# Performance work log

Hardware: AMD Instinct MI355X
Metric: run time of the kernel (lower is better)

Reference implementation:

```python
import jax, jax.numpy as jnp
import numpy as np

N, C_IN, C_OUT, K = 100000, 64, 64, 16
E = N * K
BN_EPS = 1e-5


def setup_inputs() -> dict:
    key = jax.random.key(0)
    ks = jax.random.split(key, 4)
    x = jax.random.normal(ks[0], (N, C_IN), dtype=jnp.float32)
    # knn-style edge list: each node i is the center (row) of exactly K edges
    edge_row = jnp.repeat(jnp.arange(N, dtype=jnp.int64), K)
    edge_col = jax.random.randint(ks[1], (E,), 0, N).astype(jnp.int64)
    W1 = jax.random.normal(ks[2], (2 * C_IN, C_OUT), dtype=jnp.float32) * (1.0 / np.sqrt(2 * C_IN))
    W2 = jax.random.normal(ks[3], (C_OUT, C_OUT), dtype=jnp.float32) * (1.0 / np.sqrt(C_OUT))
    return {
        'x': x, 'edge_row': edge_row, 'edge_col': edge_col,
        'W1': W1, 'b1': jnp.zeros((C_OUT,), jnp.float32),
        'g1': jnp.ones((C_OUT,), jnp.float32), 'be1': jnp.zeros((C_OUT,), jnp.float32),
        'W2': W2, 'b2': jnp.zeros((C_OUT,), jnp.float32),
        'g2': jnp.ones((C_OUT,), jnp.float32), 'be2': jnp.zeros((C_OUT,), jnp.float32),
    }


def _bn(h, gamma, beta):
    # BatchNorm1d in training mode: biased batch stats over the edge dim
    mean = jnp.mean(h, axis=0)
    var = jnp.mean(jnp.square(h - mean), axis=0)
    return (h - mean) * jax.lax.rsqrt(var + BN_EPS) * gamma + beta


def reference(x, edge_row, edge_col, W1, b1, g1, be1, W2, b2, g2, be2):
    xi = x[edge_row]                      # [E, C_in]  gather (center)
    xj = x[edge_col]                      # [E, C_in]  gather (neighbor)
    feat = jnp.concatenate([xi, xj - xi], axis=1)   # [E, 2*C_in]
    h = jax.nn.relu(_bn(feat @ W1 + b1, g1, be1))   # [E, C_out]
    h = jax.nn.relu(_bn(h @ W2 + b2, g2, be2))      # [E, C_out]
    # scatter-max back to nodes; every node has K edges so no empty segments
    out = jax.ops.segment_max(h, edge_row, num_segments=x.shape[0])
    return out
```

## Files before the change

### kernel.cpp

```cpp
#include <hip/hip_runtime.h>


#define N_NODES 100000
#define KE 16
#define E_EDGES (N_NODES * KE)
#define BN_EPS 1e-5f
#define NCHUNK (N_NODES / KE)
#define GSLOTS 16

typedef __attribute__((ext_vector_type(8))) short bf16x8;
typedef __attribute__((ext_vector_type(4))) float f32x4;
typedef __attribute__((ext_vector_type(4))) int i32x4;

#define MFMA(a, b, c) __builtin_amdgcn_mfma_f32_16x16x32_bf16((a), (b), (c), 0, 0, 0)

static __device__ __forceinline__ short bf16b(float f) {
  __bf16 h = (__bf16)f;
  return __builtin_bit_cast(short, h);
}

#if __has_builtin(__builtin_amdgcn_cvt_pk_bf16_f32)
static __device__ __forceinline__ int pk2(float a, float b) {
  return __builtin_bit_cast(int, __builtin_amdgcn_cvt_pk_bf16_f32(a, b));
}
#else
static __device__ __forceinline__ int pk2(float a, float b) {
  return (int)(unsigned short)bf16b(a) | ((int)(unsigned short)bf16b(b) << 16);
}
#endif

static __device__ __forceinline__ bf16x8 pack8(float4 a, float4 b) {
  i32x4 v = {pk2(a.x, a.y), pk2(a.z, a.w), pk2(b.x, b.y), pk2(b.z, b.w)};
  return __builtin_bit_cast(bf16x8, v);
}

static __device__ __forceinline__ float bf2f(short s) {
  unsigned u = ((unsigned)(unsigned short)s) << 16;
  return __builtin_bit_cast(float, u);
}

__global__ __launch_bounds__(256) void k_prep(const float* __restrict__ x,
                                              short* __restrict__ xb,
                                              const float* __restrict__ W1,
                                              const float* __restrict__ W2,
                                              short* __restrict__ wp1,
                                              short* __restrict__ wp2,
                                              float* __restrict__ gaccz) {
  if (blockIdx.x < 3125) {
    int g = blockIdx.x * 256 + threadIdx.x;
    const float4* x4 = (const float4*)x;
    float4 f0 = x4[2 * g], f1 = x4[2 * g + 1];
    *(bf16x8*)(xb + g * 8) = pack8(f0, f1);
    return;
  }
  if (blockIdx.x == 3131) {
    float4 z = {0.f, 0.f, 0.f, 0.f};
    for (int i = 0; i < 4; i++)
      ((float4*)gaccz)[threadIdx.x * 4 + i] = z;
    return;
  }
  int tid = (blockIdx.x - 3125) * 256 + threadIdx.x;
  if (tid < 1024) {
    int l = tid & 63, st = tid >> 6;
    int s = st >> 2, t = st & 3;
    int quad = l >> 4, n16 = l & 15;
    for (int j = 0; j < 8; j++) {
      int k = 32 * s + quad * 8 + j, c = 16 * t + n16;
      float w = (s < 2) ? (W1[k * 64 + c] - W1[(k + 64) * 64 + c])
                        : W1[k * 64 + c];
      wp1[tid * 8 + j] = bf16b(w);
    }
  } else if (tid < 1536) {
    int e = tid - 1024;
    int l = e & 63, st = e >> 6;
    int s = st >> 2, t = st & 3;
    int quad = l >> 4, n16 = l & 15;
    for (int j = 0; j < 8; j++) {
      int k = 32 * s + quad * 8 + j, c = 16 * t + n16;
      wp2[e * 8 + j] = bf16b(W2[k * 64 + c]);
    }
  }
}

static __device__ __forceinline__ void stat_acc(const f32x4 acc[4], float sacc[4],
                                                float qacc[4]) {
#pragma unroll
  for (int t = 0; t < 4; t++) {
    sacc[t] += (acc[t][0] + acc[t][1]) + (acc[t][2] + acc[t][3]);
    qacc[t] = fmaf(acc[t][0], acc[t][0],
              fmaf(acc[t][1], acc[t][1],
              fmaf(acc[t][2], acc[t][2],
              fmaf(acc[t][3], acc[t][3], qacc[t]))));
  }
}

static __device__ __forceinline__ void stat_flush(float sacc[4], float qacc[4],
                                                  int quad, int n16, float* lstat) {
#pragma unroll
  for (int t = 0; t < 4; t++) {
    float s = sacc[t], q = qacc[t];
    s += __shfl_xor(s, 16); s += __shfl_xor(s, 32);
    q += __shfl_xor(q, 16); q += __shfl_xor(q, 32);
    if (quad == 0) {
      atomicAdd(&lstat[16 * t + n16], s);
      atomicAdd(&lstat[64 + 16 * t + n16], q);
    }
  }
}

static __device__ __forceinline__ void bn_finalize(const float* __restrict__ gacc,
                                                   const float* __restrict__ g,
                                                   const float* __restrict__ be,
                                                   float* lbn, int tid) {
  if (tid < 64) {
    float s = 0.f, q = 0.f;
#pragma unroll
    for (int i = 0; i < GSLOTS; i++) {
      s += gacc[i * 128 + tid];
      q += gacc[i * 128 + 64 + tid];
    }
    float mean = s * (1.0f / E_EDGES);
    float var = q * (1.0f / E_EDGES) - mean * mean;
    float rstd = rsqrtf(var + BN_EPS);
    float a = g[tid] * rstd;
    lbn[tid] = a;
    lbn[64 + tid] = be[tid] - mean * a;
  }
}

static __device__ __forceinline__ void compute_y(const short* __restrict__ xisrc,
                                                 const short* wfl,
                                                 float* yt, int l, int quad, int n16) {
  bf16x8 a0 = *(const bf16x8*)(&xisrc[n16 * 64 + quad * 8]);
  bf16x8 a1 = *(const bf16x8*)(&xisrc[n16 * 64 + 32 + quad * 8]);
  const bf16x8* wf = (const bf16x8*)wfl;
#pragma unroll
  for (int t = 0; t < 4; t++) {
    f32x4 y = {0.f, 0.f, 0.f, 0.f};
    y = MFMA(a0, wf[(0 + t) * 64 + l], y);
    y = MFMA(a1, wf[(4 + t) * 64 + l], y);
#pragma unroll
    for (int r = 0; r < 4; r++)
      yt[(quad * 4 + r) * 64 + 16 * t + n16] = y[r];
  }
}

__global__ __launch_bounds__(256, 4) void k_pass1(const short* __restrict__ xb,
                                                  const int* __restrict__ ecol,
                                                  const bf16x8* __restrict__ wp1,
                                                  float* __restrict__ gacc) {
  __shared__ float lstat[128];
  __shared__ float yt[1024];
  __shared__ __align__(16) short wfl[8192];
  int tid = threadIdx.x;
  if (tid < 128) lstat[tid] = 0.f;
  int nb = blockIdx.x * 16;
  int wave = tid >> 6, l = tid & 63, quad = l >> 4, n16 = l & 15;
  int idx[4];
#pragma unroll
  for (int v = 0; v < 4; v++)
    idx[v] = ecol[nb * KE + (wave * 4 + v) * 16 + n16];
  bf16x8 j0[4], j1[4];
#pragma unroll
  for (int v = 0; v < 4; v++) {
    const short* pj = xb + (size_t)idx[v] * 64 + quad * 8;
    j0[v] = *(const bf16x8*)pj;
    j1[v] = *(const bf16x8*)(pj + 32);
  }
#pragma unroll
  for (int r = 0; r < 4; r++)
    ((bf16x8*)wfl)[r * 256 + tid] = wp1[r * 256 + tid];
  __syncthreads();
  const bf16x8* wf = (const bf16x8*)wfl;
  if (wave == 0) compute_y(xb + (size_t)nb * 64, wfl, yt, l, quad, n16);
  __syncthreads();
  float sacc[4] = {0.f, 0.f, 0.f, 0.f}, qacc[4] = {0.f, 0.f, 0.f, 0.f};
#pragma unroll
  for (int v = 0; v < 4; v++) {
    int p = wave * 4 + v;
    f32x4 acc[4];
#pragma unroll
    for (int t = 0; t < 4; t++) {
      float yv = yt[p * 64 + 16 * t + n16];
      f32x4 a = {yv, yv, yv, yv};
      a = MFMA(j0[v], wf[(8 + t) * 64 + l], a);
      a = MFMA(j1[v], wf[(12 + t) * 64 + l], a);
      acc[t] = a;
    }
    stat_acc(acc, sacc, qacc);
  }
  stat_flush(sacc, qacc, quad, n16, lstat);
  __syncthreads();
  if (tid < 128)
    atomicAdd(&gacc[(blockIdx.x & (GSLOTS - 1)) * 128 + tid], lstat[tid]);
}

__global__ __launch_bounds__(256, 4) void k_pass2(const short* __restrict__ xb,
                                                  const int* __restrict__ ecol,
                                                  const bf16x8* __restrict__ wp1,
                                                  const bf16x8* __restrict__ wp2,
                                                  const float* __restrict__ gacc1,
                                                  const float* __restrict__ g1,
                                                  const float* __restrict__ be1,
                                                  float* __restrict__ gacc,
                                                  short* __restrict__ hmax,
                                                  short* __restrict__ hmin) {
  __shared__ float lstat[128];
  __shared__ float lbn[128];
  __shared__ float yt[1024];
  __shared__ __align__(16) short wfl[8192];
  __shared__ __align__(16) short tiles[4][16 * 72];
  int tid = threadIdx.x;
  if (tid < 128) lstat[tid] = 0.f;
  bn_finalize(gacc1, g1, be1, lbn, tid);
  int nb = blockIdx.x * 16;
  int wave = tid >> 6, l = tid & 63, quad = l >> 4, n16 = l & 15;
  int idx[4];
#pragma unroll
  for (int v = 0; v < 4; v++)
    idx[v] = ecol[nb * KE + (wave * 4 + v) * 16 + n16];
  bf16x8 j0[4], j1[4];
#pragma unroll
  for (int v = 0; v < 4; v++) {
    const short* pj = xb + (size_t)idx[v] * 64 + quad * 8;
    j0[v] = *(const bf16x8*)pj;
    j1[v] = *(const bf16x8*)(pj + 32);
  }
#pragma unroll
  for (int r = 0; r < 4; r++)
    ((bf16x8*)wfl)[r * 256 + tid] = wp1[r * 256 + tid];
  const bf16x8* wf = (const bf16x8*)wfl;
  bf16x8 wf2[8];
#pragma unroll
  for (int u = 0; u < 8; u++) wf2[u] = wp2[u * 64 + l];
  __syncthreads();
  float a1c[4], b1c[4];
#pragma unroll
  for (int t = 0; t < 4; t++) {
    a1c[t] = lbn[16 * t + n16];
    b1c[t] = lbn[64 + 16 * t + n16];
  }
  if (wave == 0) compute_y(xb + (size_t)nb * 64, wfl, yt, l, quad, n16);
  __syncthreads();
  float sacc[4] = {0.f, 0.f, 0.f, 0.f}, qacc[4] = {0.f, 0.f, 0.f, 0.f};
  short* myt = &tiles[wave][0];
#pragma unroll
  for (int v = 0; v < 4; v++) {
    int p = wave * 4 + v;
    f32x4 acc1[4];
#pragma unroll
    for (int t = 0; t < 4; t++) {
      float yv = yt[p * 64 + 16 * t + n16];
      f32x4 a = {yv, yv, yv, yv};
      a = MFMA(j0[v], wf[(8 + t) * 64 + l], a);
      a = MFMA(j1[v], wf[(12 + t) * 64 + l], a);
      acc1[t] = a;
    }
#pragma unroll
    for (int t = 0; t < 4; t++) {
      int c = 16 * t + n16;
#pragma unroll
      for (int r = 0; r < 4; r++) {
        float h = fmaxf(fmaf(acc1[t][r], a1c[t], b1c[t]), 0.f);
        myt[(quad * 4 + r) * 72 + c] = bf16b(h);
      }
    }
    bf16x8 f0 = *(bf16x8*)(myt + n16 * 72 + quad * 8);
    bf16x8 f1 = *(bf16x8*)(myt + n16 * 72 + 32 + quad * 8);
    f32x4 acc2[4];
#pragma unroll
    for (int t = 0; t < 4; t++) {
      f32x4 a = {0.f, 0.f, 0.f, 0.f};
      a = MFMA(f0, wf2[0 + t], a);
      a = MFMA(f1, wf2[4 + t], a);
      acc2[t] = a;
    }
    stat_acc(acc2, sacc, qacc);
    float vmx[4], vmn[4];
#pragma unroll
    for (int t = 0; t < 4; t++) {
      float mx = fmaxf(fmaxf(acc2[t][0], acc2[t][1]), fmaxf(acc2[t][2], acc2[t][3]));
      float mn = fminf(fminf(acc2[t][0], acc2[t][1]), fminf(acc2[t][2], acc2[t][3]));
      mx = fmaxf(mx, __shfl_xor(mx, 16)); mx = fmaxf(mx, __shfl_xor(mx, 32));
      mn = fminf(mn, __shfl_xor(mn, 16)); mn = fminf(mn, __shfl_xor(mn, 32));
      vmx[t] = mx; vmn[t] = mn;
    }
    int n = nb + p;
    float ox = (quad == 0) ? vmx[0] : (quad == 1) ? vmx[1] : (quad == 2) ? vmx[2] : vmx[3];
    float on = (quad == 0) ? vmn[0] : (quad == 1) ? vmn[1] : (quad == 2) ? vmn[2] : vmn[3];
    hmax[(size_t)n * 64 + l] = bf16b(ox);
    hmin[(size_t)n * 64 + l] = bf16b(on);
  }
  stat_flush(sacc, qacc, quad, n16, lstat);
  __syncthreads();
  if (tid < 128)
    atomicAdd(&gacc[(blockIdx.x & (GSLOTS - 1)) * 128 + tid], lstat[tid]);
}

__global__ __launch_bounds__(256) void k_pass3(const short* __restrict__ hmax,
                                               const short* __restrict__ hmin,
                                               const float* __restrict__ gacc2,
                                               const float* __restrict__ g2,
                                               const float* __restrict__ be2,
                                               float* __restrict__ out) {
  __shared__ float lbn[128];
  int tid = threadIdx.x;
  bn_finalize(gacc2, g2, be2, lbn, tid);
  __syncthreads();
  int g = blockIdx.x * 256 + tid;
  int base = g * 4;
  int c4 = base & 63;
  short4 mx4 = *(const short4*)(hmax + base);
  short4 mn4 = *(const short4*)(hmin + base);
  float4 a4 = *(const float4*)(&lbn[c4]);
  float4 b4 = *(const float4*)(&lbn[64 + c4]);
  float4 o;
  o.x = fmaxf(a4.x >= 0.f ? fmaf(a4.x, bf2f(mx4.x), b4.x) : fmaf(a4.x, bf2f(mn4.x), b4.x), 0.f);
  o.y = fmaxf(a4.y >= 0.f ? fmaf(a4.y, bf2f(mx4.y), b4.y) : fmaf(a4.y, bf2f(mn4.y), b4.y), 0.f);
  o.z = fmaxf(a4.z >= 0.f ? fmaf(a4.z, bf2f(mx4.z), b4.z) : fmaf(a4.z, bf2f(mn4.z), b4.z), 0.f);
  o.w = fmaxf(a4.w >= 0.f ? fmaf(a4.w, bf2f(mx4.w), b4.w) : fmaf(a4.w, bf2f(mn4.w), b4.w), 0.f);
  *(float4*)(out + base) = o;
}

extern "C" void kernel_launch(void* const* d_in, const int* in_sizes, int n_in,
                              void* d_out, int out_size, void* d_ws, size_t ws_size,
                              hipStream_t stream) {
  const float* x   = (const float*)d_in[0];
  const int*   ec  = (const int*)d_in[2];
  const float* W1  = (const float*)d_in[3];
  const float* g1  = (const float*)d_in[5];
  const float* be1 = (const float*)d_in[6];
  const float* W2  = (const float*)d_in[7];
  const float* g2  = (const float*)d_in[9];
  const float* be2 = (const float*)d_in[10];
  float* out = (float*)d_out;

  char* ws = (char*)d_ws;
  bf16x8* wp1  = (bf16x8*)(ws);
  bf16x8* wp2  = (bf16x8*)(ws + 16384);
  float* gacc1 = (float*)(ws + 24576);
  float* gacc2 = (float*)(ws + 32768);
  short* xb    = (short*)(ws + 98304);
  short* hmax  = (short*)(ws + 98304 + 12800000);
  short* hmin  = (short*)(ws + 98304 + 2 * 12800000);

  hipLaunchKernelGGL(k_prep, dim3(3132), dim3(256), 0, stream, x, xb,
                     W1, W2, (short*)wp1, (short*)wp2, gacc1);
  hipLaunchKernelGGL(k_pass1, dim3(NCHUNK), dim3(256), 0, stream,
                     xb, ec, wp1, gacc1);
  hipLaunchKernelGGL(k_pass2, dim3(NCHUNK), dim3(256), 0, stream,
                     xb, ec, wp1, wp2, gacc1, g1, be1, gacc2, hmax, hmin);
  hipLaunchKernelGGL(k_pass3, dim3(6250), dim3(256), 0, stream,
                     hmax, hmin, gacc2, g2, be2, out);
}
```

Before: 219.3 us.

## Precompute per-node first-layer projections Y and Z, gather projections instead of features

Splits the first linear layer by linearity: each node's contributions Y = x·(W1a−W1b) in fp32 and Z = x·W1b in bf16 are computed once per node in a new kernel. The edge pre-activation then becomes Y[row] + Z[col], so the two edge passes no longer run first-layer MFMAs or stage W1 in shared memory. Pass 1 reduces to an elementwise add plus sum and sum-of-squares statistics, and pass 2 applies batch norm directly to the gathered Z. The cost is an extra kernel and larger intermediates (fp32 Y, bf16 Z), and rounding Z to bf16 after the matmul changes numerics slightly.

```diff
diff --git a/kernel.cpp b/kernel.cpp
--- a/kernel.cpp
+++ b/kernel.cpp
@@ -6,6 +6,7 @@
 #define E_EDGES (N_NODES * KE)
 #define BN_EPS 1e-5f
 #define NCHUNK (N_NODES / KE)
+#define NTILES (N_NODES / 16)
 #define GSLOTS 16
 
 typedef __attribute__((ext_vector_type(8))) short bf16x8;
@@ -34,32 +35,28 @@
   return __builtin_bit_cast(bf16x8, v);
 }
 
+static __device__ __forceinline__ bf16x8 pack8f(const float h[8]) {
+  i32x4 v = {pk2(h[0], h[1]), pk2(h[2], h[3]), pk2(h[4], h[5]), pk2(h[6], h[7])};
+  return __builtin_bit_cast(bf16x8, v);
+}
+
 static __device__ __forceinline__ float bf2f(short s) {
   unsigned u = ((unsigned)(unsigned short)s) << 16;
   return __builtin_bit_cast(float, u);
 }
 
-__global__ __launch_bounds__(256) void k_prep(const float* __restrict__ x,
-                                              short* __restrict__ xb,
-                                              const float* __restrict__ W1,
+__global__ __launch_bounds__(256) void k_prep(const float* __restrict__ W1,
                                               const float* __restrict__ W2,
                                               short* __restrict__ wp1,
                                               short* __restrict__ wp2,
                                               float* __restrict__ gaccz) {
-  if (blockIdx.x < 3125) {
-    int g = blockIdx.x * 256 + threadIdx.x;
-    const float4* x4 = (const float4*)x;
-    float4 f0 = x4[2 * g], f1 = x4[2 * g + 1];
-    *(bf16x8*)(xb + g * 8) = pack8(f0, f1);
-    return;
-  }
-  if (blockIdx.x == 3131) {
+  if (blockIdx.x == 6) {
     float4 z = {0.f, 0.f, 0.f, 0.f};
     for (int i = 0; i < 4; i++)
       ((float4*)gaccz)[threadIdx.x * 4 + i] = z;
     return;
   }
-  int tid = (blockIdx.x - 3125) * 256 + threadIdx.x;
+  int tid = blockIdx.x * 256 + threadIdx.x;
   if (tid < 1024) {
     int l = tid & 63, st = tid >> 6;
     int s = st >> 2, t = st & 3;
@@ -78,6 +75,34 @@
     for (int j = 0; j < 8; j++) {
       int k = 32 * s + quad * 8 + j, c = 16 * t + n16;
       wp2[e * 8 + j] = bf16b(W2[k * 64 + c]);
+    }
+  }
+}
+
+__global__ __launch_bounds__(256) void k_nodeYZ(const float* __restrict__ x,
+                                                const bf16x8* __restrict__ wp1,
+                                                float* __restrict__ Yf,
+                                                short* __restrict__ Z) {
+  int wave = threadIdx.x >> 6, l = threadIdx.x & 63, quad = l >> 4, n16 = l & 15;
+  int tile = blockIdx.x * 4 + wave;
+  if (tile >= NTILES) return;
+  const float* xr = x + (size_t)(tile * 16 + n16) * 64 + quad * 8;
+  float4 x0 = *(const float4*)xr, x1 = *(const float4*)(xr + 4);
+  float4 x2 = *(const float4*)(xr + 32), x3 = *(const float4*)(xr + 36);
+  bf16x8 a0 = pack8(x0, x1);
+  bf16x8 a1 = pack8(x2, x3);
+  f32x4 zero = {0.f, 0.f, 0.f, 0.f};
+#pragma unroll
+  for (int t = 0; t < 4; t++) {
+    f32x4 y = MFMA(a0, wp1[(0 + t) * 64 + l], zero);
+    y = MFMA(a1, wp1[(4 + t) * 64 + l], y);
+    f32x4 z = MFMA(a0, wp1[(8 + t) * 64 + l], zero);
+    z = MFMA(a1, wp1[(12 + t) * 64 + l], z);
+#pragma unroll
+    for (int r = 0; r < 4; r++) {
+      size_t row = (size_t)(tile * 16 + quad * 4 + r);
+      Yf[row * 64 + 16 * t + n16] = y[r];
+      Z[row * 64 + 16 * t + n16] = bf16b(z[r]);
     }
   }
 }
@@ -128,76 +153,69 @@
   }
 }
 
-static __device__ __forceinline__ void compute_y(const short* __restrict__ xisrc,
-                                                 const short* wfl,
-                                                 float* yt, int l, int quad, int n16) {
-  bf16x8 a0 = *(const bf16x8*)(&xisrc[n16 * 64 + quad * 8]);
-  bf16x8 a1 = *(const bf16x8*)(&xisrc[n16 * 64 + 32 + quad * 8]);
-  const bf16x8* wf = (const bf16x8*)wfl;
-#pragma unroll
-  for (int t = 0; t < 4; t++) {
-    f32x4 y = {0.f, 0.f, 0.f, 0.f};
-    y = MFMA(a0, wf[(0 + t) * 64 + l], y);
-    y = MFMA(a1, wf[(4 + t) * 64 + l], y);
-#pragma unroll
-    for (int r = 0; r < 4; r++)
-      yt[(quad * 4 + r) * 64 + 16 * t + n16] = y[r];
-  }
-}
-
-__global__ __launch_bounds__(256, 4) void k_pass1(const short* __restrict__ xb,
-                                                  const int* __restrict__ ecol,
-                                                  const bf16x8* __restrict__ wp1,
-                                                  float* __restrict__ gacc) {
+__global__ __launch_bounds__(256, 4) void k_stats1(const short* __restrict__ Z,
+                                                   const float* __restrict__ Yf,
+                                                   const int* __restrict__ ecol,
+                                                   float* __restrict__ gacc) {
   __shared__ float lstat[128];
-  __shared__ float yt[1024];
-  __shared__ __align__(16) short wfl[8192];
+  __shared__ float ytile[1024];
   int tid = threadIdx.x;
   if (tid < 128) lstat[tid] = 0.f;
   int nb = blockIdx.x * 16;
+  ((float4*)ytile)[tid] = ((const float4*)(Yf + (size_t)nb * 64))[tid];
   int wave = tid >> 6, l = tid & 63, quad = l >> 4, n16 = l & 15;
   int idx[4];
 #pragma unroll
   for (int v = 0; v < 4; v++)
     idx[v] = ecol[nb * KE + (wave * 4 + v) * 16 + n16];
-  bf16x8 j0[4], j1[4];
+  bf16x8 zf0[4], zf1[4];
 #pragma unroll
   for (int v = 0; v < 4; v++) {
-    const short* pj = xb + (size_t)idx[v] * 64 + quad * 8;
-    j0[v] = *(const bf16x8*)pj;
-    j1[v] = *(const bf16x8*)(pj + 32);
-  }
-#pragma unroll
-  for (int r = 0; r < 4; r++)
-    ((bf16x8*)wfl)[r * 256 + tid] = wp1[r * 256 + tid];
-  __syncthreads();
-  const bf16x8* wf = (const bf16x8*)wfl;
-  if (wave == 0) compute_y(xb + (size_t)nb * 64, wfl, yt, l, quad, n16);
-  __syncthreads();
-  float sacc[4] = {0.f, 0.f, 0.f, 0.f}, qacc[4] = {0.f, 0.f, 0.f, 0.f};
+    const short* pz = Z + (size_t)idx[v] * 64 + quad * 8;
+    zf0[v] = *(const bf16x8*)pz;
+    zf1[v] = *(const bf16x8*)(pz + 32);
+  }
+  __syncthreads();
+  float s0[8], q0[8], s1[8], q1[8];
+#pragma unroll
+  for (int j = 0; j < 8; j++) { s0[j] = q0[j] = s1[j] = q1[j] = 0.f; }
 #pragma unroll
   for (int v = 0; v < 4; v++) {
     int p = wave * 4 + v;
-    f32x4 acc[4];
-#pragma unroll
-    for (int t = 0; t < 4; t++) {
-      float yv = yt[p * 64 + 16 * t + n16];
-      f32x4 a = {yv, yv, yv, yv};
-      a = MFMA(j0[v], wf[(8 + t) * 64 + l], a);
-      a = MFMA(j1[v], wf[(12 + t) * 64 + l], a);
-      acc[t] = a;
-    }
-    stat_acc(acc, sacc, qacc);
-  }
-  stat_flush(sacc, qacc, quad, n16, lstat);
+    const float* yb = &ytile[p * 64 + quad * 8];
+#pragma unroll
+    for (int j = 0; j < 8; j++) {
+      float h = yb[j] + bf2f(zf0[v][j]);
+      s0[j] += h; q0[j] = fmaf(h, h, q0[j]);
+      float h2 = yb[32 + j] + bf2f(zf1[v][j]);
+      s1[j] += h2; q1[j] = fmaf(h2, h2, q1[j]);
+    }
+  }
+#pragma unroll
+  for (int j = 0; j < 8; j++) {
+#pragma unroll
+    for (int d = 1; d < 16; d <<= 1) {
+      s0[j] += __shfl_xor(s0[j], d); q0[j] += __shfl_xor(q0[j], d);
+      s1[j] += __shfl_xor(s1[j], d); q1[j] += __shfl_xor(q1[j], d);
+    }
+  }
+  if (n16 == 0) {
+#pragma unroll
+    for (int j = 0; j < 8; j++) {
+      atomicAdd(&lstat[quad * 8 + j], s0[j]);
+      atomicAdd(&lstat[64 + quad * 8 + j], q0[j]);
+      atomicAdd(&lstat[32 + quad * 8 + j], s1[j]);
+      atomicAdd(&lstat[96 + quad * 8 + j], q1[j]);
+    }
+  }
   __syncthreads();
   if (tid < 128)
     atomicAdd(&gacc[(blockIdx.x & (GSLOTS - 1)) * 128 + tid], lstat[tid]);
 }
 
-__global__ __launch_bounds__(256, 4) void k_pass2(const short* __restrict__ xb,
+__global__ __launch_bounds__(256, 4) void k_pass2(const short* __restrict__ Z,
+                                                  const float* __restrict__ Yf,
                                                   const int* __restrict__ ecol,
-                                                  const bf16x8* __restrict__ wp1,
                                                   const bf16x8* __restrict__ wp2,
                                                   const float* __restrict__ gacc1,
                                                   const float* __restrict__ g1,
@@ -207,9 +225,7 @@
                                                   short* __restrict__ hmin) {
   __shared__ float lstat[128];
   __shared__ float lbn[128];
-  __shared__ float yt[1024];
-  __shared__ __align__(16) short wfl[8192];
-  __shared__ __align__(16) short tiles[4][16 * 72];
+  __shared__ float btile[1024];
   int tid = threadIdx.x;
   if (tid < 128) lstat[tid] = 0.f;
   bn_finalize(gacc1, g1, be1, lbn, tid);
@@ -219,54 +235,38 @@
 #pragma unroll
   for (int v = 0; v < 4; v++)
     idx[v] = ecol[nb * KE + (wave * 4 + v) * 16 + n16];
-  bf16x8 j0[4], j1[4];
+  bf16x8 zf0[4], zf1[4];
 #pragma unroll
   for (int v = 0; v < 4; v++) {
-    const short* pj = xb + (size_t)idx[v] * 64 + quad * 8;
-    j0[v] = *(const bf16x8*)pj;
-    j1[v] = *(const bf16x8*)(pj + 32);
-  }
-#pragma unroll
-  for (int r = 0; r < 4; r++)
-    ((bf16x8*)wfl)[r * 256 + tid] = wp1[r * 256 + tid];
-  const bf16x8* wf = (const bf16x8*)wfl;
+    const short* pz = Z + (size_t)idx[v] * 64 + quad * 8;
+    zf0[v] = *(const bf16x8*)pz;
+    zf1[v] = *(const bf16x8*)(pz + 32);
+  }
   bf16x8 wf2[8];
 #pragma unroll
   for (int u = 0; u < 8; u++) wf2[u] = wp2[u * 64 + l];
   __syncthreads();
-  float a1c[4], b1c[4];
-#pragma unroll
-  for (int t = 0; t < 4; t++) {
-    a1c[t] = lbn[16 * t + n16];
-    b1c[t] = lbn[64 + 16 * t + n16];
-  }
-  if (wave == 0) compute_y(xb + (size_t)nb * 64, wfl, yt, l, quad, n16);
-  __syncthreads();
+  for (int i = tid; i < 1024; i += 256)
+    btile[i] = fmaf(lbn[i & 63], Yf[(size_t)nb * 64 + i], lbn[64 + (i & 63)]);
+  __syncthreads();
+  float ac0[8], ac1[8];
+#pragma unroll
+  for (int j = 0; j < 8; j++) {
+    ac0[j] = lbn[quad * 8 + j];
+    ac1[j] = lbn[32 + quad * 8 + j];
+  }
   float sacc[4] = {0.f, 0.f, 0.f, 0.f}, qacc[4] = {0.f, 0.f, 0.f, 0.f};
-  short* myt = &tiles[wave][0];
 #pragma unroll
   for (int v = 0; v < 4; v++) {
     int p = wave * 4 + v;
-    f32x4 acc1[4];
-#pragma unroll
-    for (int t = 0; t < 4; t++) {
-      float yv = yt[p * 64 + 16 * t + n16];
-      f32x4 a = {yv, yv, yv, yv};
-      a = MFMA(j0[v], wf[(8 + t) * 64 + l], a);
-      a = MFMA(j1[v], wf[(12 + t) * 64 + l], a);
-      acc1[t] = a;
-    }
-#pragma unroll
-    for (int t = 0; t < 4; t++) {
-      int c = 16 * t + n16;
-#pragma unroll
-      for (int r = 0; r < 4; r++) {
-        float h = fmaxf(fmaf(acc1[t][r], a1c[t], b1c[t]), 0.f);
-        myt[(quad * 4 + r) * 72 + c] = bf16b(h);
-      }
-    }
-    bf16x8 f0 = *(bf16x8*)(myt + n16 * 72 + quad * 8);
-    bf16x8 f1 = *(bf16x8*)(myt + n16 * 72 + 32 + quad * 8);
+    const float* bb = &btile[p * 64 + quad * 8];
+    float h0[8], h1[8];
+#pragma unroll
+    for (int j = 0; j < 8; j++) {
+      h0[j] = fmaxf(fmaf(ac0[j], bf2f(zf0[v][j]), bb[j]), 0.f);
+      h1[j] = fmaxf(fmaf(ac1[j], bf2f(zf1[v][j]), bb[32 + j]), 0.f);
+    }
+    bf16x8 f0 = pack8f(h0), f1 = pack8f(h1);
     f32x4 acc2[4];
 #pragma unroll
     for (int t = 0; t < 4; t++) {
@@ -340,16 +340,19 @@
   bf16x8* wp2  = (bf16x8*)(ws + 16384);
   float* gacc1 = (float*)(ws + 24576);
   float* gacc2 = (float*)(ws + 32768);
-  short* xb    = (short*)(ws + 98304);
-  short* hmax  = (short*)(ws + 98304 + 12800000);
-  short* hmin  = (short*)(ws + 98304 + 2 * 12800000);
-
-  hipLaunchKernelGGL(k_prep, dim3(3132), dim3(256), 0, stream, x, xb,
+  float* Yf    = (float*)(ws + 98304);
+  short* Zb    = (short*)(ws + 98304 + 25600000);
+  short* hmax  = (short*)(ws + 98304 + 25600000 + 12800000);
+  short* hmin  = (short*)(ws + 98304 + 25600000 + 2 * 12800000);
+
+  hipLaunchKernelGGL(k_prep, dim3(7), dim3(256), 0, stream,
                      W1, W2, (short*)wp1, (short*)wp2, gacc1);
-  hipLaunchKernelGGL(k_pass1, dim3(NCHUNK), dim3(256), 0, stream,
-                     xb, ec, wp1, gacc1);
+  hipLaunchKernelGGL(k_nodeYZ, dim3((NTILES + 3) / 4), dim3(256), 0, stream,
+                     x, wp1, Yf, Zb);
+  hipLaunchKernelGGL(k_stats1, dim3(NCHUNK), dim3(256), 0, stream,
+                     Zb, Yf, ec, gacc1);
   hipLaunchKernelGGL(k_pass2, dim3(NCHUNK), dim3(256), 0, stream,
-                     xb, ec, wp1, wp2, gacc1, g1, be1, gacc2, hmax, hmin);
+                     Zb, Yf, ec, wp2, gacc1, g1, be1, gacc2, hmax, hmin);
   hipLaunchKernelGGL(k_pass3, dim3(6250), dim3(256), 0, stream,
                      hmax, hmin, gacc2, g2, be2, out);
 }
```

Result: slower. 237.2 us (+8.1%).
